# Kernel optimization log

Hardware: AMD Instinct MI355X
Metric: run time of the kernel (lower is better)

## Reference

```python
import jax, jax.numpy as jnp
import numpy as np

HEIGHT, WIDTH, NUM_FRAMES, DIM = 64, 64, 16, 1280
GRIDS = [(8, 32, 32), (16, 16, 16), (4, 48, 48), (1, 64, 64)]  # ragged (t,h,w) per sample


def _sincos_1d(embed_dim, t_size):
    # matches get_1d_sincos_pos_embed_from_grid
    omega = np.arange(embed_dim // 2, dtype=np.float32) / (embed_dim / 2.0)
    omega = 1.0 / (10000.0 ** omega)
    pos = np.arange(t_size, dtype=np.float32)
    out = np.einsum('m,d->md', pos, omega)
    return np.concatenate([np.sin(out), np.cos(out)], axis=1).astype(np.float32)  # [t, dim]


def setup_inputs() -> dict:
    key = jax.random.key(0)
    k1, k2 = jax.random.split(key)
    total_tokens = sum(t * h * w for t, h, w in GRIDS)  # 25600
    x = jax.random.normal(k1, (total_tokens, DIM), dtype=jnp.float32)
    weight = jax.random.normal(k2, (HEIGHT, WIDTH, DIM), dtype=jnp.float32)  # learnable 2D pos emb
    time_weight = jnp.asarray(_sincos_1d(DIM, NUM_FRAMES))  # [num_frames, dim] sincos buffer
    grid_thws = np.asarray(GRIDS, dtype=np.int64)  # static per-sample (t,h,w)
    return {"x": x, "weight": weight, "time_weight": time_weight, "grid_thws": grid_thws}


def reference(x, weight, time_weight, grid_thws):
    H, W, D = weight.shape
    grids = np.asarray(grid_thws).tolist()  # static metadata; loop is over ragged samples
    pos_embs = []
    for t, h, w in grids:
        if (h, w) == (H, W):
            pe2d = weight.reshape(-1, D)  # [h*w, D]
        else:
            # torch path: fp32 bicubic interpolation of [H,W,D] -> [h,w,D]
            pe2d = jax.image.resize(weight.astype(jnp.float32), (h, w, D),
                                    method='bicubic').astype(x.dtype).reshape(-1, D)
        if t == 1:
            pe3d = pe2d
        else:
            # broadcast-add temporal sincos embedding: [t,1,D] + [1,h*w,D]
            pe3d = (pe2d[None, :, :] + time_weight[:t, None, :]).reshape(-1, D)
        pos_embs.append(pe3d)
    return x + jnp.concatenate(pos_embs, axis=0)
```

## Files before the change

### kernel.cpp

```cpp
#include <hip/hip_runtime.h>


#define PE32_OFF 0
#define PE16_OFF 1310720
#define PE48_OFF 1638400

typedef float f32x4 __attribute__((ext_vector_type(4)));

__device__ __forceinline__ float keys_cubic(float x) {
    x = fabsf(x);
    if (x >= 2.0f) return 0.0f;
    if (x >= 1.0f) return ((-0.5f * x + 2.5f) * x - 4.0f) * x + 2.0f;
    return ((1.5f * x - 2.5f) * x) * x + 1.0f;
}

__device__ __forceinline__ void tap_params(int o, int out_size,
                                           int& i0, int& n, float& sf,
                                           float& inv_ks, float& inv_sum) {
    float inv_scale = 64.0f / (float)out_size;
    float ks = inv_scale;
    float radius = 2.0f * ks;
    sf = ((float)o + 0.5f) * inv_scale - 0.5f;
    int lo = (int)ceilf(sf - radius); if (lo < 0) lo = 0;
    int hi = (int)floorf(sf + radius); if (hi > 63) hi = 63;
    n = hi - lo + 1;
    i0 = lo;
    inv_ks = 1.0f / ks;
    float sum = 0.0f;
    for (int k = 0; k < n; ++k)
        sum += keys_cubic((sf - (float)(lo + k)) * inv_ks);
    inv_sum = 1.0f / sum;
}

#define TMP_STRIDE 68
#define MAXTAP 17
__global__ __launch_bounds__(256) void resize2d_kernel(const float* __restrict__ weight,
                                                       float* __restrict__ ws) {
    int td  = blockIdx.x % 20;
    int row = blockIdx.x / 20;
    int out_h, out_w, oy; float* pe_base;
    if (row < 32)      { out_h = 32; out_w = 32; oy = row;      pe_base = ws + PE32_OFF; }
    else if (row < 48) { out_h = 16; out_w = 16; oy = row - 32; pe_base = ws + PE16_OFF; }
    else               { out_h = 48; out_w = 48; oy = row - 48; pe_base = ws + PE48_OFF; }
    int d0 = td * 64;

    __shared__ float tmp[64 * TMP_STRIDE];
    __shared__ float vcoef[MAXTAP];
    __shared__ int   vmeta[2];
    __shared__ float hcoef[48][MAXTAP + 1];
    __shared__ int   hj0[48];
    __shared__ int   hn[48];

    int tid = threadIdx.x;

    if (tid == 192) {
        int i0, n; float sf, ik, is;
        tap_params(oy, out_h, i0, n, sf, ik, is);
        vmeta[0] = i0; vmeta[1] = n;
        for (int k = 0; k < n; ++k)
            vcoef[k] = keys_cubic((sf - (float)(i0 + k)) * ik) * is;
    }
    if (tid < out_w) {
        int j0, n; float sf, ik, is;
        tap_params(tid, out_w, j0, n, sf, ik, is);
        hj0[tid] = j0; hn[tid] = n;
        for (int k = 0; k < n; ++k)
            hcoef[tid][k] = keys_cubic((sf - (float)(j0 + k)) * ik) * is;
    }
    __syncthreads();

    int i0 = vmeta[0], nh = vmeta[1];
    for (int item = tid; item < 1024; item += 256) {
        int x  = item >> 4;
        int f4 = item & 15;
        const float* src = weight + (size_t)x * 1280 + d0 + (f4 << 2);
        float4 acc = make_float4(0.f, 0.f, 0.f, 0.f);
        for (int k = 0; k < nh; ++k) {
            float c = vcoef[k];
            float4 v = *(const float4*)(src + (size_t)(i0 + k) * (64 * 1280));
            acc.x += c * v.x; acc.y += c * v.y; acc.z += c * v.z; acc.w += c * v.w;
        }
        *(float4*)&tmp[x * TMP_STRIDE + (f4 << 2)] = acc;
    }
    __syncthreads();

    int nitems = out_w << 4;
    for (int item = tid; item < nitems; item += 256) {
        int ox = item >> 4;
        int f4 = item & 15;
        int j0 = hj0[ox], nw = hn[ox];
        float4 acc = make_float4(0.f, 0.f, 0.f, 0.f);
        for (int k = 0; k < nw; ++k) {
            float c = hcoef[ox][k];
            float4 v = *(const float4*)&tmp[(j0 + k) * TMP_STRIDE + (f4 << 2)];
            acc.x += c * v.x; acc.y += c * v.y; acc.z += c * v.z; acc.w += c * v.w;
        }
        *(float4*)(pe_base + (size_t)(oy * out_w + ox) * 1280 + d0 + (f4 << 2)) = acc;
    }
}

__global__ __launch_bounds__(256) void add_pe_kernel(const float* __restrict__ x,
                                                     const float* __restrict__ weight,
                                                     const float* __restrict__ tw,
                                                     const float* __restrict__ ws,
                                                     float* __restrict__ out) {
    int p = blockIdx.x * 256 + threadIdx.x;
    int token = p / 160;
    int d = (p - token * 160) << 3;

    const float* pe;
    int frame;
    if (token < 8192) {
        frame = token >> 10;
        int px = token & 1023;
        pe = ws + PE32_OFF + (size_t)px * 1280;
    } else if (token < 12288) {
        int l = token - 8192;
        frame = l >> 8;
        int px = l & 255;
        pe = ws + PE16_OFF + (size_t)px * 1280;
    } else if (token < 21504) {
        int l = token - 12288;
        frame = l / 2304;
        int px = l - frame * 2304;
        pe = ws + PE48_OFF + (size_t)px * 1280;
    } else {
        int l = token - 21504;
        frame = -1;
        pe = weight + (size_t)l * 1280;
    }

    size_t off = (size_t)token * 1280 + d;
    f32x4 x0 = __builtin_nontemporal_load((const f32x4*)(x + off));
    f32x4 x1 = __builtin_nontemporal_load((const f32x4*)(x + off + 4));
    f32x4 p0 = *(const f32x4*)(pe + d);
    f32x4 p1 = *(const f32x4*)(pe + d + 4);
    f32x4 o0 = x0 + p0;
    f32x4 o1 = x1 + p1;
    if (frame >= 0) {
        f32x4 t0 = *(const f32x4*)(tw + (size_t)frame * 1280 + d);
        f32x4 t1 = *(const f32x4*)(tw + (size_t)frame * 1280 + d + 4);
        o0 += t0;
        o1 += t1;
    }
    __builtin_nontemporal_store(o0, (f32x4*)(out + off));
    __builtin_nontemporal_store(o1, (f32x4*)(out + off + 4));
}

extern "C" void kernel_launch(void* const* d_in, const int* in_sizes, int n_in,
                              void* d_out, int out_size, void* d_ws, size_t ws_size,
                              hipStream_t stream) {
    const float* x      = (const float*)d_in[0];
    const float* weight = (const float*)d_in[1];
    const float* tw     = (const float*)d_in[2];
    float* ws  = (float*)d_ws;
    float* out = (float*)d_out;

    hipLaunchKernelGGL(resize2d_kernel, dim3(1920), dim3(256), 0, stream, weight, ws);
    hipLaunchKernelGGL(add_pe_kernel, dim3(16000), dim3(256), 0, stream, x, weight, tw, ws, out);
}
```

Before: 265.4 us.

## Fuse bicubic resize and positional-embedding add into one kernel

Merges the resize kernel and the add kernel into one launch. Each block computes one resized PE row slice for 64 channels into LDS, then streams x and writes out for every frame that reuses that row. This removes the workspace write and re-read of the interpolated embeddings and one kernel launch. In exchange the grid is smaller and uneven (3200 blocks, some looping over 16 frames), LDS use per block grows, and the nontemporal load/store hints are dropped.

```diff
diff --git a/kernel.cpp b/kernel.cpp
--- a/kernel.cpp
+++ b/kernel.cpp
@@ -1,11 +1,5 @@
 #include <hip/hip_runtime.h>
 
-
-#define PE32_OFF 0
-#define PE16_OFF 1310720
-#define PE48_OFF 1638400
-
-typedef float f32x4 __attribute__((ext_vector_type(4)));
 
 __device__ __forceinline__ float keys_cubic(float x) {
     x = fabsf(x);
@@ -33,118 +27,107 @@
 }
 
 #define TMP_STRIDE 68
+#define PE_STRIDE  68
 #define MAXTAP 17
-__global__ __launch_bounds__(256) void resize2d_kernel(const float* __restrict__ weight,
-                                                       float* __restrict__ ws) {
-    int td  = blockIdx.x % 20;
-    int row = blockIdx.x / 20;
-    int out_h, out_w, oy; float* pe_base;
-    if (row < 32)      { out_h = 32; out_w = 32; oy = row;      pe_base = ws + PE32_OFF; }
-    else if (row < 48) { out_h = 16; out_w = 16; oy = row - 32; pe_base = ws + PE16_OFF; }
-    else               { out_h = 48; out_w = 48; oy = row - 48; pe_base = ws + PE48_OFF; }
-    int d0 = td * 64;
 
+__global__ __launch_bounds__(256) void fused_pe_kernel(const float* __restrict__ x,
+                                                       const float* __restrict__ weight,
+                                                       const float* __restrict__ tw,
+                                                       float* __restrict__ out) {
     __shared__ float tmp[64 * TMP_STRIDE];
+    __shared__ float pe_lds[48 * PE_STRIDE];
     __shared__ float vcoef[MAXTAP];
     __shared__ int   vmeta[2];
     __shared__ float hcoef[48][MAXTAP + 1];
     __shared__ int   hj0[48];
     __shared__ int   hn[48];
 
+    int td  = blockIdx.x % 20;
+    int row = blockIdx.x / 20;
+    int d0  = td * 64;
     int tid = threadIdx.x;
 
-    if (tid == 192) {
-        int i0, n; float sf, ik, is;
-        tap_params(oy, out_h, i0, n, sf, ik, is);
-        vmeta[0] = i0; vmeta[1] = n;
-        for (int k = 0; k < n; ++k)
-            vcoef[k] = keys_cubic((sf - (float)(i0 + k)) * ik) * is;
+    if (row >= 96) {
+        int oy = row - 96;
+        const float* wrow = weight + (size_t)oy * 64 * 1280 + d0;
+        size_t obase = (size_t)(21504 + oy * 64) * 1280 + d0;
+        for (int item = tid; item < 1024; item += 256) {
+            int ox = item >> 4, f4 = item & 15;
+            size_t xo = obase + (size_t)ox * 1280 + (f4 << 2);
+            float4 xv = *(const float4*)(x + xo);
+            float4 pv = *(const float4*)(wrow + (size_t)ox * 1280 + (f4 << 2));
+            float4 o = make_float4(xv.x + pv.x, xv.y + pv.y, xv.z + pv.z, xv.w + pv.w);
+            *(float4*)(out + xo) = o;
+        }
+    } else {
+        int out_h, out_w, oy, t, tok_off, hw;
+        if (row < 32)      { out_h = 32; out_w = 32; oy = row;      t = 8;  tok_off = 0;     hw = 1024; }
+        else if (row < 48) { out_h = 16; out_w = 16; oy = row - 32; t = 16; tok_off = 8192;  hw = 256;  }
+        else               { out_h = 48; out_w = 48; oy = row - 48; t = 4;  tok_off = 12288; hw = 2304; }
+
+        if (tid == 192) {
+            int i0, n; float sf, ik, is;
+            tap_params(oy, out_h, i0, n, sf, ik, is);
+            vmeta[0] = i0; vmeta[1] = n;
+            for (int k = 0; k < n; ++k)
+                vcoef[k] = keys_cubic((sf - (float)(i0 + k)) * ik) * is;
+        }
+        if (tid < out_w) {
+            int j0, n; float sf, ik, is;
+            tap_params(tid, out_w, j0, n, sf, ik, is);
+            hj0[tid] = j0; hn[tid] = n;
+            for (int k = 0; k < n; ++k)
+                hcoef[tid][k] = keys_cubic((sf - (float)(j0 + k)) * ik) * is;
+        }
+        __syncthreads();
+
+        int i0 = vmeta[0], nh = vmeta[1];
+        for (int item = tid; item < 1024; item += 256) {
+            int sx = item >> 4;
+            int f4 = item & 15;
+            const float* src = weight + (size_t)sx * 1280 + d0 + (f4 << 2);
+            float4 acc = make_float4(0.f, 0.f, 0.f, 0.f);
+            for (int k = 0; k < nh; ++k) {
+                float c = vcoef[k];
+                float4 v = *(const float4*)(src + (size_t)(i0 + k) * (64 * 1280));
+                acc.x += c * v.x; acc.y += c * v.y; acc.z += c * v.z; acc.w += c * v.w;
+            }
+            *(float4*)&tmp[sx * TMP_STRIDE + (f4 << 2)] = acc;
+        }
+        __syncthreads();
+
+        for (int item = tid; item < (out_w << 4); item += 256) {
+            int ox = item >> 4;
+            int f4 = item & 15;
+            int j0 = hj0[ox], nw = hn[ox];
+            float4 acc = make_float4(0.f, 0.f, 0.f, 0.f);
+            for (int k = 0; k < nw; ++k) {
+                float c = hcoef[ox][k];
+                float4 v = *(const float4*)&tmp[(j0 + k) * TMP_STRIDE + (f4 << 2)];
+                acc.x += c * v.x; acc.y += c * v.y; acc.z += c * v.z; acc.w += c * v.w;
+            }
+            *(float4*)&pe_lds[ox * PE_STRIDE + (f4 << 2)] = acc;
+        }
+        __syncthreads();
+
+        size_t rbase = (size_t)(tok_off + oy * out_w) * 1280 + d0;
+        int nitems = out_w << 4;
+        for (int f = 0; f < t; ++f) {
+            size_t fbase = rbase + (size_t)f * hw * 1280;
+            const float* twf = tw + (size_t)f * 1280 + d0;
+            for (int item = tid; item < nitems; item += 256) {
+                int ox = item >> 4;
+                int f4 = item & 15;
+                size_t xo = fbase + (size_t)ox * 1280 + (f4 << 2);
+                float4 xv = *(const float4*)(x + xo);
+                float4 pv = *(const float4*)&pe_lds[ox * PE_STRIDE + (f4 << 2)];
+                float4 tv = *(const float4*)(twf + (f4 << 2));
+                float4 o = make_float4(xv.x + pv.x + tv.x, xv.y + pv.y + tv.y,
+                                       xv.z + pv.z + tv.z, xv.w + pv.w + tv.w);
+                *(float4*)(out + xo) = o;
+            }
+        }
     }
-    if (tid < out_w) {
-        int j0, n; float sf, ik, is;
-        tap_params(tid, out_w, j0, n, sf, ik, is);
-        hj0[tid] = j0; hn[tid] = n;
-        for (int k = 0; k < n; ++k)
-            hcoef[tid][k] = keys_cubic((sf - (float)(j0 + k)) * ik) * is;
-    }
-    __syncthreads();
-
-    int i0 = vmeta[0], nh = vmeta[1];
-    for (int item = tid; item < 1024; item += 256) {
-        int x  = item >> 4;
-        int f4 = item & 15;
-        const float* src = weight + (size_t)x * 1280 + d0 + (f4 << 2);
-        float4 acc = make_float4(0.f, 0.f, 0.f, 0.f);
-        for (int k = 0; k < nh; ++k) {
-            float c = vcoef[k];
-            float4 v = *(const float4*)(src + (size_t)(i0 + k) * (64 * 1280));
-            acc.x += c * v.x; acc.y += c * v.y; acc.z += c * v.z; acc.w += c * v.w;
-        }
-        *(float4*)&tmp[x * TMP_STRIDE + (f4 << 2)] = acc;
-    }
-    __syncthreads();
-
-    int nitems = out_w << 4;
-    for (int item = tid; item < nitems; item += 256) {
-        int ox = item >> 4;
-        int f4 = item & 15;
-        int j0 = hj0[ox], nw = hn[ox];
-        float4 acc = make_float4(0.f, 0.f, 0.f, 0.f);
-        for (int k = 0; k < nw; ++k) {
-            float c = hcoef[ox][k];
-            float4 v = *(const float4*)&tmp[(j0 + k) * TMP_STRIDE + (f4 << 2)];
-            acc.x += c * v.x; acc.y += c * v.y; acc.z += c * v.z; acc.w += c * v.w;
-        }
-        *(float4*)(pe_base + (size_t)(oy * out_w + ox) * 1280 + d0 + (f4 << 2)) = acc;
-    }
-}
-
-__global__ __launch_bounds__(256) void add_pe_kernel(const float* __restrict__ x,
-                                                     const float* __restrict__ weight,
-                                                     const float* __restrict__ tw,
-                                                     const float* __restrict__ ws,
-                                                     float* __restrict__ out) {
-    int p = blockIdx.x * 256 + threadIdx.x;
-    int token = p / 160;
-    int d = (p - token * 160) << 3;
-
-    const float* pe;
-    int frame;
-    if (token < 8192) {
-        frame = token >> 10;
-        int px = token & 1023;
-        pe = ws + PE32_OFF + (size_t)px * 1280;
-    } else if (token < 12288) {
-        int l = token - 8192;
-        frame = l >> 8;
-        int px = l & 255;
-        pe = ws + PE16_OFF + (size_t)px * 1280;
-    } else if (token < 21504) {
-        int l = token - 12288;
-        frame = l / 2304;
-        int px = l - frame * 2304;
-        pe = ws + PE48_OFF + (size_t)px * 1280;
-    } else {
-        int l = token - 21504;
-        frame = -1;
-        pe = weight + (size_t)l * 1280;
-    }
-
-    size_t off = (size_t)token * 1280 + d;
-    f32x4 x0 = __builtin_nontemporal_load((const f32x4*)(x + off));
-    f32x4 x1 = __builtin_nontemporal_load((const f32x4*)(x + off + 4));
-    f32x4 p0 = *(const f32x4*)(pe + d);
-    f32x4 p1 = *(const f32x4*)(pe + d + 4);
-    f32x4 o0 = x0 + p0;
-    f32x4 o1 = x1 + p1;
-    if (frame >= 0) {
-        f32x4 t0 = *(const f32x4*)(tw + (size_t)frame * 1280 + d);
-        f32x4 t1 = *(const f32x4*)(tw + (size_t)frame * 1280 + d + 4);
-        o0 += t0;
-        o1 += t1;
-    }
-    __builtin_nontemporal_store(o0, (f32x4*)(out + off));
-    __builtin_nontemporal_store(o1, (f32x4*)(out + off + 4));
 }
 
 extern "C" void kernel_launch(void* const* d_in, const int* in_sizes, int n_in,
@@ -153,9 +136,8 @@
     const float* x      = (const float*)d_in[0];
     const float* weight = (const float*)d_in[1];
     const float* tw     = (const float*)d_in[2];
-    float* ws  = (float*)d_ws;
     float* out = (float*)d_out;
 
-    hipLaunchKernelGGL(resize2d_kernel, dim3(1920), dim3(256), 0, stream, weight, ws);
-    hipLaunchKernelGGL(add_pe_kernel, dim3(16000), dim3(256), 0, stream, x, weight, tw, ws, out);
+    hipLaunchKernelGGL(fused_pe_kernel, dim3(3200), dim3(256), 0, stream,
+                       x, weight, tw, out);
 }
```

After: 262.9 us. No clear change (-1.0%).
